# Kernel tuning notes

Hardware: AMD Instinct MI355X
Metric: run time of the kernel (lower is better)

Reference implementation:

```python
import jax, jax.numpy as jnp
import numpy as np

# Dimensions matching init_kwargs
O = 4096   # out_features
I = 4096   # in_features
R = 32     # svd_rank
G = 64     # n_groups
GS = I // G  # group_size = 64
NBITS = 4
NUM_BYTES = O * I * NBITS // 8


def setup_inputs() -> dict:
    key = jax.random.key(0)
    ks = jax.random.split(key, 7)
    return {
        "x": jax.random.normal(ks[0], (1, 4096, I), dtype=jnp.float32),
        # bit-packed int4 weights, two nibbles per byte (stored as int32 holding 0..255)
        "w_packed": jax.random.randint(ks[1], (NUM_BYTES,), 0, 256, dtype=jnp.int32),
        "svd_up": jax.random.normal(ks[2], (O, R), dtype=jnp.float32) * 0.02,
        "svd_down": jax.random.normal(ks[3], (R, I), dtype=jnp.float32) * 0.02,
        "scale": jax.random.uniform(ks[4], (O, G, 1), dtype=jnp.float32, minval=0.001, maxval=0.02),
        "zero_point": jax.random.uniform(ks[5], (O, G, 1), dtype=jnp.float32, minval=0.0, maxval=15.0),
        "bias": jax.random.normal(ks[6], (O,), dtype=jnp.float32) * 0.01,
    }


def _dequantize(w_packed, svd_up, svd_down, scale, zero_point):
    # Unpack two 4-bit values per byte (low nibble first).
    low = w_packed & 0xF
    high = (w_packed >> 4) & 0xF
    w_q = jnp.stack([low, high], axis=-1).reshape(O, G, GS).astype(jnp.float32)
    # Per-group affine dequant: (q - zero) * scale, then SVD low-rank correction.
    W = ((w_q - zero_point) * scale).reshape(O, I)
    return W + svd_up @ svd_down  # [O, I]


def reference(x, w_packed, svd_up, svd_down, scale, zero_point, bias):
    # forward_int8 path (tokens > 16, int8_matmul=True)
    W_f = _dequantize(w_packed, svd_up, svd_down, scale, zero_point).T  # [I, O]
    xm = x.reshape(-1, I)  # [N, I]
    # Dynamic per-row activation quant
    scale_x = jnp.max(jnp.abs(xm), axis=1, keepdims=True) / 127.0  # [N, 1]
    x_q = jnp.clip(jnp.round(xm / scale_x), -128, 127).astype(jnp.int8)
    # Dynamic per-column weight quant
    scale_w = jnp.max(jnp.abs(W_f), axis=0, keepdims=True) / 127.0  # [1, O]
    W_q = jnp.clip(jnp.round(W_f / scale_w), -128, 127).astype(jnp.int8)
    # int8 GEMM with int32 accumulation, then dequant scales + bias
    acc = jnp.matmul(x_q.astype(jnp.int32), W_q.astype(jnp.int32))  # [N, O] int32
    out = acc.astype(jnp.float32) * scale_x * scale_w + bias
    return out.reshape(*x.shape[:-1], O)
```

## Files before the change

### kernel.cpp

```cpp
#include <hip/hip_runtime.h>
#include <cstdint>
#include <cstddef>

#define I_DIM 4096
#define O_DIM 4096
#define RNK 32
#define NGRP 64
#define N_TOK 4096

typedef int v4i  __attribute__((ext_vector_type(4)));
typedef int v16i __attribute__((ext_vector_type(16)));

__device__ __forceinline__ int clamp_i8(float v) {
    int q = (int)rintf(v);
    q = q < -128 ? -128 : q;
    q = q > 127 ? 127 : q;
    return q;
}

#define BO 4
#define W_BLOCKS (O_DIM / BO)

__device__ __forceinline__ void quant_w_body(
    const int* __restrict__ w_packed, const float* __restrict__ svd_up,
    const float* __restrict__ svd_down, const float* __restrict__ scale,
    const float* __restrict__ zp, char* __restrict__ w_q,
    float* __restrict__ scale_w, int blk)
{
    __shared__ float s_sc[BO][NGRP];
    __shared__ float s_zp[BO][NGRP];
    __shared__ float s_red[BO][4];
    __shared__ float s_sw[BO];

    const int tid = threadIdx.x;
    const int o0 = blk * BO;

    for (int t = tid; t < BO * NGRP; t += 256) {
        s_sc[t >> 6][t & 63] = scale[(size_t)(o0 + (t >> 6)) * NGRP + (t & 63)];
        s_zp[t >> 6][t & 63] = zp[(size_t)(o0 + (t >> 6)) * NGRP + (t & 63)];
    }
    __syncthreads();

    float W[4][BO][4];

#pragma unroll
    for (int jq = 0; jq < 4; jq++) {
        const int q = tid + 256 * jq;
        const int g = q >> 4;
#pragma unroll
        for (int ro = 0; ro < BO; ro++) {
            const int2 b2 = *(const int2*)&w_packed[(size_t)(o0 + ro) * (I_DIM / 2) + 2 * q];
            const float sc = s_sc[ro][g], z = s_zp[ro][g];
            W[jq][ro][0] = ((float)(b2.x & 0xF) - z) * sc;
            W[jq][ro][1] = ((float)((b2.x >> 4) & 0xF) - z) * sc;
            W[jq][ro][2] = ((float)(b2.y & 0xF) - z) * sc;
            W[jq][ro][3] = ((float)((b2.y >> 4) & 0xF) - z) * sc;
        }
    }

#pragma unroll 2
    for (int r = 0; r < RNK; r++) {
        float u[BO];
#pragma unroll
        for (int ro = 0; ro < BO; ro++)
            u[ro] = svd_up[(size_t)(o0 + ro) * RNK + r];
        float4 d[4];
#pragma unroll
        for (int jq = 0; jq < 4; jq++)
            d[jq] = *(const float4*)&svd_down[(size_t)r * I_DIM + 4 * (tid + 256 * jq)];
#pragma unroll
        for (int jq = 0; jq < 4; jq++)
#pragma unroll
            for (int ro = 0; ro < BO; ro++) {
                W[jq][ro][0] += u[ro] * d[jq].x;
                W[jq][ro][1] += u[ro] * d[jq].y;
                W[jq][ro][2] += u[ro] * d[jq].z;
                W[jq][ro][3] += u[ro] * d[jq].w;
            }
    }

    float vmax[BO];
#pragma unroll
    for (int ro = 0; ro < BO; ro++) vmax[ro] = 0.0f;
#pragma unroll
    for (int jq = 0; jq < 4; jq++)
#pragma unroll
        for (int ro = 0; ro < BO; ro++)
            vmax[ro] = fmaxf(vmax[ro],
                fmaxf(fmaxf(fabsf(W[jq][ro][0]), fabsf(W[jq][ro][1])),
                      fmaxf(fabsf(W[jq][ro][2]), fabsf(W[jq][ro][3]))));

    const int lane = tid & 63, wv = tid >> 6;
#pragma unroll
    for (int ro = 0; ro < BO; ro++) {
        float m = vmax[ro];
        for (int off = 32; off > 0; off >>= 1)
            m = fmaxf(m, __shfl_down(m, off, 64));
        if (lane == 0) s_red[ro][wv] = m;
    }
    __syncthreads();
    if (tid < BO) {
        const float m = fmaxf(fmaxf(s_red[tid][0], s_red[tid][1]),
                              fmaxf(s_red[tid][2], s_red[tid][3]));
        const float sw = m / 127.0f;
        scale_w[o0 + tid] = sw;
        s_sw[tid] = sw;
    }
    __syncthreads();

    float inv[BO];
#pragma unroll
    for (int ro = 0; ro < BO; ro++) inv[ro] = 1.0f / s_sw[ro];

#pragma unroll
    for (int jq = 0; jq < 4; jq++) {
        const int q = tid + 256 * jq;
#pragma unroll
        for (int ro = 0; ro < BO; ro++) {
            const int q0 = clamp_i8(W[jq][ro][0] * inv[ro]);
            const int q1 = clamp_i8(W[jq][ro][1] * inv[ro]);
            const int q2 = clamp_i8(W[jq][ro][2] * inv[ro]);
            const int q3 = clamp_i8(W[jq][ro][3] * inv[ro]);
            ((int*)w_q)[(size_t)(o0 + ro) * (I_DIM / 4) + q] =
                (q0 & 0xFF) | ((q1 & 0xFF) << 8) | ((q2 & 0xFF) << 16) | ((q3 & 0xFF) << 24);
        }
    }
}

__device__ __forceinline__ void quant_x_body(
    const float* __restrict__ x, char* __restrict__ x_q,
    float* __restrict__ scale_x, int n)
{
    const int tid = threadIdx.x;
    const float4* xr = (const float4*)(x + (size_t)n * I_DIM);
    float4 v[4];
    float m = 0.0f;
#pragma unroll
    for (int j = 0; j < 4; j++) {
        v[j] = xr[tid + 256 * j];
        m = fmaxf(m, fmaxf(fmaxf(fabsf(v[j].x), fabsf(v[j].y)),
                           fmaxf(fabsf(v[j].z), fabsf(v[j].w))));
    }
    __shared__ float s_red[4];
    __shared__ float s_sx;
    for (int off = 32; off > 0; off >>= 1)
        m = fmaxf(m, __shfl_down(m, off, 64));
    if ((tid & 63) == 0) s_red[tid >> 6] = m;
    __syncthreads();
    if (tid == 0) {
        const float mm = fmaxf(fmaxf(s_red[0], s_red[1]),
                               fmaxf(s_red[2], s_red[3]));
        const float sx = mm / 127.0f;
        scale_x[n] = sx;
        s_sx = sx;
    }
    __syncthreads();
    const float sx = s_sx;
    int* outw = (int*)(x_q + (size_t)n * I_DIM);
#pragma unroll
    for (int j = 0; j < 4; j++) {
        const int q0 = clamp_i8(v[j].x / sx);
        const int q1 = clamp_i8(v[j].y / sx);
        const int q2 = clamp_i8(v[j].z / sx);
        const int q3 = clamp_i8(v[j].w / sx);
        outw[tid + 256 * j] =
            (q0 & 0xFF) | ((q1 & 0xFF) << 8) | ((q2 & 0xFF) << 16) | ((q3 & 0xFF) << 24);
    }
}

__global__ __launch_bounds__(256, 4) void prep_kernel(
    const int* __restrict__ w_packed, const float* __restrict__ svd_up,
    const float* __restrict__ svd_down, const float* __restrict__ scale,
    const float* __restrict__ zp, char* __restrict__ w_q,
    float* __restrict__ scale_w,
    const float* __restrict__ x, char* __restrict__ x_q,
    float* __restrict__ scale_x)
{
    if (blockIdx.x < W_BLOCKS)
        quant_w_body(w_packed, svd_up, svd_down, scale, zp, w_q, scale_w, blockIdx.x);
    else
        quant_x_body(x, x_q, scale_x, blockIdx.x - W_BLOCKS);
}

#define TBM 256
#define TBN 256
#define TBK 64
#define NKT (I_DIM / TBK)

__device__ __forceinline__ void stage_tile(const char* __restrict__ src, int row0,
                                           int t, char* lds_mat, int tid)
{
#pragma unroll
    for (int uu = 0; uu < 2; uu++) {
        const int c = tid + uu * 512;
        const int row = c >> 2;
        const int kc = (c & 3) ^ ((row >> 1) & 3);
        const char* g = src + (size_t)(row0 + row) * I_DIM + t * TBK + kc * 16;
        __builtin_amdgcn_global_load_lds(
            (const __attribute__((address_space(1))) unsigned int*)g,
            (__attribute__((address_space(3))) unsigned int*)(lds_mat + c * 16),
            16, 0, 0);
    }
}

#define READ_FRAGS(P) do {                                                  \
    _Pragma("unroll")                                                       \
    for (int mt = 0; mt < 4; mt++) {                                        \
        const int row = wm * 128 + mt * 32 + l31;                           \
        const int kc = ((P) * 2 + h) ^ ((row >> 1) & 3);                    \
        af[mt] = *(const v4i*)(Ac + row * TBK + kc * 16);                   \
    }                                                                       \
    _Pragma("unroll")                                                       \
    for (int nt = 0; nt < 2; nt++) {                                        \
        const int row = wn * 64 + nt * 32 + l31;                            \
        const int kc = ((P) * 2 + h) ^ ((row >> 1) & 3);                    \
        bf[nt] = *(const v4i*)(Bc + row * TBK + kc * 16);                   \
    }                                                                       \
} while (0)

#define MFMA_CLUSTER() do {                                                 \
    __builtin_amdgcn_s_setprio(1);                                          \
    _Pragma("unroll")                                                       \
    for (int mt = 0; mt < 4; mt++)                                          \
        _Pragma("unroll")                                                   \
        for (int nt = 0; nt < 2; nt++)                                      \
            acc[mt][nt] = __builtin_amdgcn_mfma_i32_32x32x32_i8(            \
                af[mt], bf[nt], acc[mt][nt], 0, 0, 0);                      \
    __builtin_amdgcn_s_setprio(0);                                          \
} while (0)

__global__ __launch_bounds__(512, 2) void gemm_i8_kernel(
    const char* __restrict__ x_q, const char* __restrict__ w_q,
    const float* __restrict__ scale_x, const float* __restrict__ scale_w,
    const float* __restrict__ bias, float* __restrict__ out)
{
    __shared__ v4i smem4[3 * 2 * 1024];
    char* lds = (char*)smem4;

    const int tid = threadIdx.x;
    const int id = blockIdx.x;
    const int xcd = id & 7;
    const int s = id >> 3;
    const int bm0 = (s & 15) * TBM;
    const int bn0 = (xcd * 2 + (s >> 4)) * TBN;

    const int lane = tid & 63, wv = tid >> 6;
    const int wm = wv >> 2, wn = wv & 3;
    const int l31 = lane & 31, h = lane >> 5;

    v16i acc[4][2];
#pragma unroll
    for (int mt = 0; mt < 4; mt++)
#pragma unroll
        for (int nt = 0; nt < 2; nt++)
            acc[mt][nt] = (v16i)(0);

    stage_tile(x_q, bm0, 0, lds + 0 * 16384, tid);
    stage_tile(w_q, bn0, 0, lds + 1 * 16384, tid);
    stage_tile(x_q, bm0, 1, lds + 2 * 16384, tid);
    stage_tile(w_q, bn0, 1, lds + 3 * 16384, tid);
    asm volatile("s_waitcnt vmcnt(4)" ::: "memory");
    __builtin_amdgcn_s_barrier();

    int cb = 0, nb = 2;
    for (int t = 0; t < NKT; ++t) {
        char* Ac = lds + (2 * cb + 0) * 16384;
        char* Bc = lds + (2 * cb + 1) * 16384;
        const bool pf = (t + 2 < NKT);
        v4i af[4], bf[2];

        if (pf) stage_tile(x_q, bm0, t + 2, lds + (2 * nb + 0) * 16384, tid);
        READ_FRAGS(0);
        __builtin_amdgcn_s_barrier();
        MFMA_CLUSTER();
        __builtin_amdgcn_s_barrier();

        if (pf) stage_tile(w_q, bn0, t + 2, lds + (2 * nb + 1) * 16384, tid);
        READ_FRAGS(1);
        __builtin_amdgcn_s_barrier();
        MFMA_CLUSTER();
        if (t < NKT - 2)       asm volatile("s_waitcnt vmcnt(4)" ::: "memory");
        else if (t == NKT - 2) asm volatile("s_waitcnt vmcnt(0)" ::: "memory");
        if (t < NKT - 1) __builtin_amdgcn_s_barrier();

        cb = (cb == 2) ? 0 : cb + 1;
        nb = (nb == 2) ? 0 : nb + 1;
    }

#pragma unroll
    for (int mt = 0; mt < 4; mt++) {
        const int rbase = bm0 + wm * 128 + mt * 32 + 4 * h;
        float sx[16];
#pragma unroll
        for (int reg = 0; reg < 16; reg++)
            sx[reg] = scale_x[rbase + (reg & 3) + 8 * (reg >> 2)];
#pragma unroll
        for (int nt = 0; nt < 2; nt++) {
            const int oc = bn0 + wn * 64 + nt * 32 + l31;
            const float sw = scale_w[oc];
            const float bs = bias[oc];
#pragma unroll
            for (int reg = 0; reg < 16; reg++) {
                const int rr = rbase + (reg & 3) + 8 * (reg >> 2);
                out[(size_t)rr * O_DIM + oc] =
                    (float)acc[mt][nt][reg] * sx[reg] * sw + bs;
            }
        }
    }
}

extern "C" void kernel_launch(void* const* d_in, const int* in_sizes, int n_in,
                              void* d_out, int out_size, void* d_ws, size_t ws_size,
                              hipStream_t stream) {
    const float* x        = (const float*)d_in[0];
    const int*   w_packed = (const int*)d_in[1];
    const float* svd_up   = (const float*)d_in[2];
    const float* svd_down = (const float*)d_in[3];
    const float* scale    = (const float*)d_in[4];
    const float* zp       = (const float*)d_in[5];
    const float* bias     = (const float*)d_in[6];
    float* out = (float*)d_out;

    char* ws = (char*)d_ws;
    char*  w_q     = ws;
    char*  x_q     = ws + ((size_t)16 << 20);
    float* scale_w = (float*)(ws + ((size_t)32 << 20));
    float* scale_x = (float*)(ws + ((size_t)32 << 20) + 16384);

    prep_kernel<<<W_BLOCKS + N_TOK, 256, 0, stream>>>(
        w_packed, svd_up, svd_down, scale, zp, w_q, scale_w, x, x_q, scale_x);
    gemm_i8_kernel<<<(N_TOK / TBM) * (O_DIM / TBN), 512, 0, stream>>>(
        x_q, w_q, scale_x, scale_w, bias, out);
}
```

Before: 254.7 us.

## Double-buffer LDS fragments in registers and cut barriers per k-step to one

Restructures the int8 GEMM main loop so that register fragments for the next half-tile are read from LDS while the MFMAs on the current fragments run, using two register fragment sets (a0/b0 and a1/b1). Each k-iteration now has a single barrier instead of four, with explicit vmcnt/lgkmcnt waits before it. The aim is to hide LDS read latency behind MFMA work and cut synchronisation overhead. In exchange it raises VGPR pressure under launch_bounds(512,2). It also depends on the hand-placed waits to avoid LDS overwrite races, since the W-tile prefetch is now issued after the first MFMA cluster.

```diff
diff --git a/kernel.cpp b/kernel.cpp
--- a/kernel.cpp
+++ b/kernel.cpp
@@ -203,29 +203,31 @@
     }
 }
 
-#define READ_FRAGS(P) do {                                                  \
+#define READ_FRAGS(AF, BF, BUF, P) do {                                     \
+    char* Ac_ = (BUF);                                                      \
+    char* Bc_ = (BUF) + 16384;                                              \
     _Pragma("unroll")                                                       \
     for (int mt = 0; mt < 4; mt++) {                                        \
         const int row = wm * 128 + mt * 32 + l31;                           \
         const int kc = ((P) * 2 + h) ^ ((row >> 1) & 3);                    \
-        af[mt] = *(const v4i*)(Ac + row * TBK + kc * 16);                   \
+        AF[mt] = *(const v4i*)(Ac_ + row * TBK + kc * 16);                  \
     }                                                                       \
     _Pragma("unroll")                                                       \
     for (int nt = 0; nt < 2; nt++) {                                        \
         const int row = wn * 64 + nt * 32 + l31;                            \
         const int kc = ((P) * 2 + h) ^ ((row >> 1) & 3);                    \
-        bf[nt] = *(const v4i*)(Bc + row * TBK + kc * 16);                   \
+        BF[nt] = *(const v4i*)(Bc_ + row * TBK + kc * 16);                  \
     }                                                                       \
 } while (0)
 
-#define MFMA_CLUSTER() do {                                                 \
+#define MFMA_CLUSTER(AF, BF) do {                                           \
     __builtin_amdgcn_s_setprio(1);                                          \
     _Pragma("unroll")                                                       \
     for (int mt = 0; mt < 4; mt++)                                          \
         _Pragma("unroll")                                                   \
         for (int nt = 0; nt < 2; nt++)                                      \
             acc[mt][nt] = __builtin_amdgcn_mfma_i32_32x32x32_i8(            \
-                af[mt], bf[nt], acc[mt][nt], 0, 0, 0);                      \
+                AF[mt], BF[nt], acc[mt][nt], 0, 0, 0);                      \
     __builtin_amdgcn_s_setprio(0);                                          \
 } while (0)
 
@@ -255,33 +257,35 @@
         for (int nt = 0; nt < 2; nt++)
             acc[mt][nt] = (v16i)(0);
 
+    v4i a0[4], b0[2], a1[4], b1[2];
+
     stage_tile(x_q, bm0, 0, lds + 0 * 16384, tid);
     stage_tile(w_q, bn0, 0, lds + 1 * 16384, tid);
     stage_tile(x_q, bm0, 1, lds + 2 * 16384, tid);
     stage_tile(w_q, bn0, 1, lds + 3 * 16384, tid);
     asm volatile("s_waitcnt vmcnt(4)" ::: "memory");
-    __builtin_amdgcn_s_barrier();
+    asm volatile("s_barrier" ::: "memory");
+    READ_FRAGS(a0, b0, lds + 0 * 32768, 0);
 
     int cb = 0, nb = 2;
     for (int t = 0; t < NKT; ++t) {
-        char* Ac = lds + (2 * cb + 0) * 16384;
-        char* Bc = lds + (2 * cb + 1) * 16384;
+        char* bufc = lds + cb * 32768;
         const bool pf = (t + 2 < NKT);
-        v4i af[4], bf[2];
-
-        if (pf) stage_tile(x_q, bm0, t + 2, lds + (2 * nb + 0) * 16384, tid);
-        READ_FRAGS(0);
-        __builtin_amdgcn_s_barrier();
-        MFMA_CLUSTER();
-        __builtin_amdgcn_s_barrier();
-
-        if (pf) stage_tile(w_q, bn0, t + 2, lds + (2 * nb + 1) * 16384, tid);
-        READ_FRAGS(1);
-        __builtin_amdgcn_s_barrier();
-        MFMA_CLUSTER();
-        if (t < NKT - 2)       asm volatile("s_waitcnt vmcnt(4)" ::: "memory");
-        else if (t == NKT - 2) asm volatile("s_waitcnt vmcnt(0)" ::: "memory");
-        if (t < NKT - 1) __builtin_amdgcn_s_barrier();
+
+        if (pf) stage_tile(x_q, bm0, t + 2, lds + nb * 32768, tid);
+        READ_FRAGS(a1, b1, bufc, 1);
+        MFMA_CLUSTER(a0, b0);
+        if (pf) stage_tile(w_q, bn0, t + 2, lds + nb * 32768 + 16384, tid);
+
+        if (t < NKT - 1) {
+            if (t < NKT - 2) asm volatile("s_waitcnt vmcnt(4)" ::: "memory");
+            else             asm volatile("s_waitcnt vmcnt(0)" ::: "memory");
+            asm volatile("s_waitcnt lgkmcnt(0)" ::: "memory");
+            asm volatile("s_barrier" ::: "memory");
+            char* bufn = lds + ((cb == 2) ? 0 : cb + 1) * 32768;
+            READ_FRAGS(a0, b0, bufn, 0);
+        }
+        MFMA_CLUSTER(a1, b1);
 
         cb = (cb == 2) ? 0 : cb + 1;
         nb = (nb == 2) ? 0 : nb + 1;
```

After: 244.5 us. 4.0% less time.
